# Performance work log

Hardware: AMD Instinct MI355X
Metric: run time of the kernel (lower is better)

Reference implementation:

```python
import jax, jax.numpy as jnp
import numpy as np

ATTN_SCALE = 0.12
HEAD_DIM = 128


def _rms_norm(x):
    # F.rms_norm with no weight; eps defaults to machine eps of dtype
    eps = jnp.asarray(jnp.finfo(x.dtype).eps, x.dtype)
    return x * jax.lax.rsqrt(jnp.mean(x * x, axis=-1, keepdims=True) + eps)


def _rope(x):
    # x: [B, T, H, D]; standard rotary over (first-half, second-half) pairs
    T, D = x.shape[1], x.shape[-1]
    half = D // 2
    inv_freq = 1.0 / (10000.0 ** (jnp.arange(half, dtype=jnp.float32) / half))
    ang = jnp.arange(T, dtype=jnp.float32)[:, None] * inv_freq[None, :]  # [T, half]
    cos = jnp.cos(ang)[None, :, None, :].astype(x.dtype)
    sin = jnp.sin(ang)[None, :, None, :].astype(x.dtype)
    x1, x2 = x[..., :half], x[..., half:]
    return jnp.concatenate([x1 * cos - x2 * sin, x1 * sin + x2 * cos], axis=-1)


def setup_inputs() -> dict:
    key = jax.random.key(0)
    ks = jax.random.split(key, 4)
    B, T, dim, H, hd = 4, 2048, 1024, 8, HEAD_DIM
    hdim = H * hd
    std = 0.5 * dim ** (-0.5)
    bound = (3.0 ** 0.5) * std
    return {
        "x": jax.random.normal(ks[0], (B, T, dim), jnp.float32),
        "ve": jax.random.normal(ks[1], (B, T, hdim), jnp.float32),
        "qkv_w": jax.random.uniform(ks[2], (3, hdim, dim), jnp.float32, -bound, bound),
        "lambdas": jnp.array([0.5, 0.5], jnp.float32),
        "c_proj_w": jax.random.normal(ks[3], (dim, hdim), jnp.float32) * (hdim ** -0.5),
        "c_proj_b": jnp.zeros((dim,), jnp.float32),
    }


def reference(x, ve, qkv_w, lambdas, c_proj_w, c_proj_b):
    B, T, dim = x.shape
    hdim = qkv_w.shape[1]
    hd = HEAD_DIM
    H = hdim // hd
    # fused QKV projection: [B,T,3,H,hd]
    qkv = jnp.einsum('btd,ehd->bteh', x, qkv_w.reshape(3 * hdim, dim).reshape(3 * H, hd, dim).reshape(3 * hdim // hd, hd, dim))
    qkv = jnp.einsum('btd,fd->btf', x, qkv_w.reshape(3 * hdim, dim)).reshape(B, T, 3, H, hd)
    q, k, v = qkv[:, :, 0], qkv[:, :, 1], qkv[:, :, 2]  # each [B,T,H,hd]
    q, k = _rms_norm(q), _rms_norm(k)
    q, k = _rope(q), _rope(k)
    v = lambdas[0] * v + lambdas[1] * ve.reshape(B, T, H, hd)
    # causal SDPA with custom scale
    scores = jnp.einsum('bthd,bshd->bhts', q, k) * ATTN_SCALE  # [B,H,T,T]
    causal = jnp.tril(jnp.ones((T, T), dtype=bool))
    scores = jnp.where(causal[None, None], scores, jnp.finfo(scores.dtype).min)
    p = jax.nn.softmax(scores, axis=-1)
    y = jnp.einsum('bhts,bshd->bthd', p, v).reshape(B, T, hdim)
    return y @ c_proj_w.T + c_proj_b
```

## Files before the change

### kernel.cpp

```cpp
#include <hip/hip_runtime.h>
#include <math.h>

typedef unsigned short u16;
typedef short bf16x8 __attribute__((ext_vector_type(8)));
typedef u16 u16x2 __attribute__((ext_vector_type(2)));
typedef u16 u16x4 __attribute__((ext_vector_type(4)));
typedef u16 u16x8 __attribute__((ext_vector_type(8)));
typedef float f32x2 __attribute__((ext_vector_type(2)));
typedef float f32x4 __attribute__((ext_vector_type(4)));
typedef float f32x16 __attribute__((ext_vector_type(16)));

typedef __attribute__((address_space(1))) const void gvoid_t;
typedef __attribute__((address_space(3))) void lvoid_t;

__device__ __forceinline__ u16 f2bf(float f) {
  union { float f; unsigned u; } v; v.f = f;
  unsigned r = v.u + 0x7fffu + ((v.u >> 16) & 1u);
  return (u16)(r >> 16);
}
__device__ __forceinline__ float bf2f(u16 h) {
  union { unsigned u; float f; } v; v.u = ((unsigned)h) << 16;
  return v.f;
}
__device__ __forceinline__ f32x4 mfma16(bf16x8 a, bf16x8 b, f32x4 c) {
  return __builtin_amdgcn_mfma_f32_16x16x32_bf16(a, b, c, 0, 0, 0);
}
__device__ __forceinline__ f32x16 mfma32(bf16x8 a, bf16x8 b, f32x16 c) {
  return __builtin_amdgcn_mfma_f32_32x32x16_bf16(a, b, c, 0, 0, 0);
}
__device__ __forceinline__ void gload_lds16(const void* g, void* l) {
  __builtin_amdgcn_global_load_lds((gvoid_t*)g, (lvoid_t*)l, 16, 0, 0);
}
__device__ __forceinline__ unsigned cvtpk_bf16(float lo, float hi) {
  unsigned r;
  asm("v_cvt_pk_bf16_f32 %0, %1, %2" : "=v"(r) : "v"(lo), "v"(hi));
  return r;
}
__device__ __forceinline__ void pswap32(unsigned& a, unsigned& b) {
  asm("v_permlane32_swap_b32 %0, %1" : "+v"(a), "+v"(b));
}

__global__ __launch_bounds__(256) void cvt_bf16_kernel(const float* __restrict__ in,
                                                       u16* __restrict__ out, int n4) {
  int i = blockIdx.x * 256 + threadIdx.x;
  if (i >= n4) return;
  f32x4 v = *(const f32x4*)(in + (size_t)i * 4);
  u16x4 o;
  o[0] = f2bf(v[0]); o[1] = f2bf(v[1]); o[2] = f2bf(v[2]); o[3] = f2bf(v[3]);
  *(u16x4*)(out + (size_t)i * 4) = o;
}

__global__ __launch_bounds__(256) void rope_tab_kernel(float* __restrict__ ct,
                                                       float* __restrict__ st) {
  int i = blockIdx.x * 256 + threadIdx.x;
  int t = i >> 6, j = i & 63;
  float inv = powf(10000.f, -(float)j * (1.0f / 64.0f));
  float ang = (float)t * inv;
  ct[i] = cosf(ang);
  st[i] = sinf(ang);
}

template <int OUTF32>
__global__ __launch_bounds__(256) void gemm_bt_kernel(
    const u16* __restrict__ A, const u16* __restrict__ B, void* __restrict__ C,
    const float* __restrict__ bias, int M, int N, int K, int ntn) {
  constexpr int BK = 64;
  __shared__ u16 Alds[128 * BK];
  __shared__ u16 Blds[128 * BK];
  int bid = blockIdx.x;
  int per_g = 8 * ntn;
  int g = bid / per_g, ing = bid % per_g;
  int bm = g * 8 + (ing & 7), bn = ing >> 3;
  size_t m0 = (size_t)bm * 128, n0 = (size_t)bn * 128;
  int tid = threadIdx.x, wid = tid >> 6, lane = tid & 63;
  int wr = wid >> 1, wc = wid & 1, l15 = lane & 15, l4 = lane >> 4;
  int srow = lane >> 3, sch = lane & 7;

  f32x4 acc[4][4];
#pragma unroll
  for (int a = 0; a < 4; a++)
#pragma unroll
    for (int b2 = 0; b2 < 4; b2++) acc[a][b2] = f32x4{0.f, 0.f, 0.f, 0.f};

  int nk = K >> 6;
  for (int kt = 0; kt < nk; ++kt) {
    int k0 = kt << 6;
    __syncthreads();
    const u16* ga = A + (m0 + 32 * wid + srow) * K + k0 + sch * 8;
    const u16* gb = B + (n0 + 32 * wid + srow) * K + k0 + sch * 8;
#pragma unroll
    for (int c = 0; c < 4; c++) {
      gload_lds16(ga + (size_t)(8 * c) * K, &Alds[(32 * wid + 8 * c) * BK]);
      gload_lds16(gb + (size_t)(8 * c) * K, &Blds[(32 * wid + 8 * c) * BK]);
    }
    __syncthreads();
#pragma unroll
    for (int kk = 0; kk < 2; kk++) {
      bf16x8 af[4], bfr[4];
#pragma unroll
      for (int mi = 0; mi < 4; mi++)
        af[mi] = *(const bf16x8*)&Alds[(64 * wr + 16 * mi + l15) * BK + kk * 32 + 8 * l4];
#pragma unroll
      for (int ni = 0; ni < 4; ni++)
        bfr[ni] = *(const bf16x8*)&Blds[(64 * wc + 16 * ni + l15) * BK + kk * 32 + 8 * l4];
#pragma unroll
      for (int mi = 0; mi < 4; mi++)
#pragma unroll
        for (int ni = 0; ni < 4; ni++)
          acc[mi][ni] = mfma16(af[mi], bfr[ni], acc[mi][ni]);
    }
  }
#pragma unroll
  for (int mi = 0; mi < 4; mi++) {
#pragma unroll
    for (int ni = 0; ni < 4; ni++) {
      size_t row = m0 + 64 * wr + 16 * mi + 4 * l4;
      size_t col = n0 + 64 * wc + 16 * ni + l15;
#pragma unroll
      for (int i = 0; i < 4; i++) {
        float v = acc[mi][ni][i];
        if constexpr (OUTF32) {
          ((float*)C)[(row + i) * N + col] = v + bias[col];
        } else {
          ((u16*)C)[(row + i) * N + col] = f2bf(v);
        }
      }
    }
  }
}

__global__ __launch_bounds__(256) void transform_kernel(
    const u16* __restrict__ qkv, const float* __restrict__ ve,
    const float* __restrict__ lam, const float* __restrict__ ct,
    const float* __restrict__ st, u16* __restrict__ qn, u16* __restrict__ kn,
    u16* __restrict__ vt) {
  constexpr int T = 2048, HD = 128;
  __shared__ u16 vtile[64][132];
  int tt = blockIdx.x, bh = blockIdx.y;
  int b = bh >> 3, h = bh & 7;
  int tid = threadIdx.x, wid = tid >> 6, lane = tid & 63;
  float l0 = lam[0], l1 = lam[1];
  int d0 = 2 * lane;
  float sgn = (lane < 32) ? -1.f : 1.f;
#pragma unroll 1
  for (int j = 0; j < 16; ++j) {
    int tl = wid * 16 + j;
    int t = tt * 64 + tl;
    size_t base = ((size_t)(b * T + t)) * 3072 + h * HD + d0;
    u16x2 qraw = *(const u16x2*)(qkv + base);
    u16x2 kraw = *(const u16x2*)(qkv + base + 1024);
    u16x2 vraw = *(const u16x2*)(qkv + base + 2048);
    f32x2 vef = *(const f32x2*)(ve + ((size_t)(b * T + t)) * 1024 + h * HD + d0);
    float q0 = bf2f(qraw[0]), q1 = bf2f(qraw[1]);
    float k0 = bf2f(kraw[0]), k1 = bf2f(kraw[1]);
    float sq = q0 * q0 + q1 * q1, sk = k0 * k0 + k1 * k1;
#pragma unroll
    for (int m = 1; m < 64; m <<= 1) {
      sq += __shfl_xor(sq, m);
      sk += __shfl_xor(sk, m);
    }
    float qs = rsqrtf(sq * (1.f / 128.f) + 1.1920929e-7f);
    float ks = rsqrtf(sk * (1.f / 128.f) + 1.1920929e-7f);
    q0 *= qs; q1 *= qs; k0 *= ks; k1 *= ks;
    int jj = d0 & 63;
    f32x2 c2 = *(const f32x2*)(ct + t * 64 + jj);
    f32x2 s2 = *(const f32x2*)(st + t * 64 + jj);
    float q0p = __shfl_xor(q0, 32), q1p = __shfl_xor(q1, 32);
    float k0p = __shfl_xor(k0, 32), k1p = __shfl_xor(k1, 32);
    u16x2 oq, ok;
    oq[0] = f2bf(q0 * c2[0] + sgn * q0p * s2[0]);
    oq[1] = f2bf(q1 * c2[1] + sgn * q1p * s2[1]);
    ok[0] = f2bf(k0 * c2[0] + sgn * k0p * s2[0]);
    ok[1] = f2bf(k1 * c2[1] + sgn * k1p * s2[1]);
    size_t orow = ((size_t)bh * T + t) * HD + d0;
    *(u16x2*)(qn + orow) = oq;
    *(u16x2*)(kn + orow) = ok;
    vtile[tl][d0] = f2bf(l0 * bf2f(vraw[0]) + l1 * vef[0]);
    vtile[tl][d0 + 1] = f2bf(l0 * bf2f(vraw[1]) + l1 * vef[1]);
  }
  __syncthreads();
#pragma unroll
  for (int it = 0; it < 4; ++it) {
    int ci = it * 256 + tid;
    int d = ci >> 3, c8 = ci & 7;
    u16x8 o;
#pragma unroll
    for (int u = 0; u < 8; u++) o[u] = vtile[c8 * 8 + u][d];
    *(u16x8*)(vt + ((size_t)bh * HD + d) * T + tt * 64 + c8 * 8) = o;
  }
}

__global__ __launch_bounds__(256, 2) void attn_kernel(
    const u16* __restrict__ Qn, const u16* __restrict__ Kn,
    const u16* __restrict__ Vt, u16* __restrict__ Y) {
  constexpr int T = 2048;
  __shared__ u16 Klds[2][64 * 128];
  __shared__ u16 Vlds[2][128 * 64];
  int bid = blockIdx.x;
  int s = 15 - (bid >> 5);
  int bh = bid & 31;
  int b = bh >> 3, h = bh & 7;
  int tid = threadIdx.x, wid = tid >> 6, lane = tid & 63;
  int l31 = lane & 31, hh = lane >> 5;
  const u16* Qb = Qn + (size_t)bh * T * 128;
  const u16* Kb = Kn + (size_t)bh * T * 128;
  const u16* Vb = Vt + (size_t)bh * 128 * T;
  int q0w = s * 128 + wid * 32;
  int qmaxw = q0w + 31;
  int ktend = 2 * s + 2;
  int qg = q0w + l31;

  bf16x8 qf[8];
  {
    const u16* qr = Qb + (size_t)(q0w + l31) * 128 + 8 * hh;
#pragma unroll
    for (int ks = 0; ks < 8; ks++) qf[ks] = *(const bf16x8*)(qr + 16 * ks);
  }
  f32x16 acc[4];
#pragma unroll
  for (int mt = 0; mt < 4; mt++)
#pragma unroll
    for (int r = 0; r < 16; r++) acc[mt][r] = 0.f;
  float m_run = -1e30f, l_run = 0.f;

  auto stage = [&](int buf, int kt) {
#pragma unroll
    for (int it = 0; it < 4; ++it) {
      int id = wid * 256 + it * 64 + lane;
      int r = id >> 4, c = id & 15;
      gload_lds16(Kb + (size_t)(kt * 64 + r) * 128 + 8 * (c ^ (r & 7)),
                  &Klds[buf][(size_t)(wid * 256 + it * 64) * 8]);
      int rv = id >> 3, cv = id & 7;
      gload_lds16(Vb + (size_t)rv * T + kt * 64 + 8 * (cv ^ (rv & 7)),
                  &Vlds[buf][(size_t)(wid * 256 + it * 64) * 8]);
    }
  };

  stage(0, 0);
  __syncthreads();

  for (int kt = 0; kt < ktend; ++kt) {
    int cur = kt & 1;
    if (kt + 1 < ktend) stage(cur ^ 1, kt + 1);
    if (kt * 64 <= qmaxw) {
      const char* kb = (const char*)&Klds[cur][0];
      const char* vb = (const char*)&Vlds[cur][0];
      int rswz = (l31 & 7) << 4;
      f32x16 st0, st1;
#pragma unroll
      for (int r = 0; r < 16; r++) { st0[r] = 0.f; st1[r] = 0.f; }
#pragma unroll
      for (int ks = 0; ks < 8; ks++) {
        bf16x8 kf0 = *(const bf16x8*)(kb + ((l31 * 256 + 32 * ks + 16 * hh) ^ rswz));
        bf16x8 kf1 = *(const bf16x8*)(kb + (((32 + l31) * 256 + 32 * ks + 16 * hh) ^ rswz));
        st0 = mfma32(kf0, qf[ks], st0);
        st1 = mfma32(kf1, qf[ks], st1);
      }
      bool edge = (kt == (qmaxw >> 6));
      if (edge) {
#pragma unroll
        for (int r = 0; r < 16; r++) {
          int kvb = kt * 64 + (r & 3) + 8 * (r >> 2) + 4 * hh;
          st0[r] = (kvb > qg) ? -1e30f : st0[r] * 0.12f;
          st1[r] = (kvb + 32 > qg) ? -1e30f : st1[r] * 0.12f;
        }
      } else {
#pragma unroll
        for (int r = 0; r < 16; r++) { st0[r] *= 0.12f; st1[r] *= 0.12f; }
      }
      float m8[8];
#pragma unroll
      for (int r = 0; r < 8; r++)
        m8[r] = fmaxf(fmaxf(st0[r], st0[r + 8]), fmaxf(st1[r], st1[r + 8]));
#pragma unroll
      for (int r = 0; r < 4; r++) m8[r] = fmaxf(m8[r], m8[r + 4]);
      float pm = fmaxf(fmaxf(m8[0], m8[1]), fmaxf(m8[2], m8[3]));
      pm = fmaxf(pm, __shfl_xor(pm, 32));
      float mnew = fmaxf(m_run, pm);
      float alpha = __expf(m_run - mnew);
      m_run = mnew;
      float sa = 0.f, sb = 0.f, sc = 0.f, sd = 0.f;
#pragma unroll
      for (int r = 0; r < 4; r++) {
        st0[r]      = __expf(st0[r]      - mnew); sa += st0[r];
        st0[r + 4]  = __expf(st0[r + 4]  - mnew); sb += st0[r + 4];
        st0[r + 8]  = __expf(st0[r + 8]  - mnew); sc += st0[r + 8];
        st0[r + 12] = __expf(st0[r + 12] - mnew); sd += st0[r + 12];
        st1[r]      = __expf(st1[r]      - mnew); sa += st1[r];
        st1[r + 4]  = __expf(st1[r + 4]  - mnew); sb += st1[r + 4];
        st1[r + 8]  = __expf(st1[r + 8]  - mnew); sc += st1[r + 8];
        st1[r + 12] = __expf(st1[r + 12] - mnew); sd += st1[r + 12];
      }
      float ps = (sa + sb) + (sc + sd);
      ps += __shfl_xor(ps, 32);
      l_run = l_run * alpha + ps;
#pragma unroll
      for (int mt = 0; mt < 4; mt++)
#pragma unroll
        for (int r = 0; r < 16; r++) acc[mt][r] *= alpha;
      unsigned pA0[4], pB0[4], pA1[4], pB1[4];
#pragma unroll
      for (int rr = 0; rr < 4; rr++) {
        pA0[rr] = cvtpk_bf16(st0[4 * rr], st0[4 * rr + 1]);
        pB0[rr] = cvtpk_bf16(st0[4 * rr + 2], st0[4 * rr + 3]);
        pA1[rr] = cvtpk_bf16(st1[4 * rr], st1[4 * rr + 1]);
        pB1[rr] = cvtpk_bf16(st1[4 * rr + 2], st1[4 * rr + 3]);
      }
      bf16x8 pf[4];
#pragma unroll
      for (int ks2 = 0; ks2 < 4; ks2++) {
        int k1 = ks2 & 1;
        unsigned a0, b0, a1, b1;
        if (ks2 < 2) { a0 = pA0[2 * k1]; b0 = pA0[2 * k1 + 1]; a1 = pB0[2 * k1]; b1 = pB0[2 * k1 + 1]; }
        else         { a0 = pA1[2 * k1]; b0 = pA1[2 * k1 + 1]; a1 = pB1[2 * k1]; b1 = pB1[2 * k1 + 1]; }
        pswap32(a0, b0);
        pswap32(a1, b1);
        union { unsigned w[4]; bf16x8 v; } u;
        u.w[0] = a0; u.w[1] = a1; u.w[2] = b0; u.w[3] = b1;
        pf[ks2] = u.v;
      }
#pragma unroll
      for (int mt = 0; mt < 4; mt++) {
        int row = 32 * mt + l31;
#pragma unroll
        for (int ks2 = 0; ks2 < 4; ks2++) {
          bf16x8 vf = *(const bf16x8*)(vb + ((row * 128 + 32 * ks2 + 16 * hh) ^ rswz));
          acc[mt] = mfma32(vf, pf[ks2], acc[mt]);
        }
      }
    }
    __syncthreads();
  }
  float linv = 1.f / l_run;
  size_t yrow = (size_t)b * T + q0w + l31;
  u16* yp = Y + yrow * 1024 + h * 128;
#pragma unroll
  for (int mt = 0; mt < 4; mt++) {
#pragma unroll
    for (int rr = 0; rr < 4; rr++) {
      u16x4 o;
#pragma unroll
      for (int i = 0; i < 4; i++) o[i] = f2bf(acc[mt][4 * rr + i] * linv);
      *(u16x4*)(yp + 32 * mt + 8 * rr + 4 * hh) = o;
    }
  }
}

extern "C" void kernel_launch(void* const* d_in, const int* in_sizes, int n_in,
                              void* d_out, int out_size, void* d_ws, size_t ws_size,
                              hipStream_t stream) {
  (void)in_sizes; (void)n_in; (void)out_size; (void)ws_size;
  const float* x = (const float*)d_in[0];
  const float* ve = (const float*)d_in[1];
  const float* qkvw = (const float*)d_in[2];
  const float* lam = (const float*)d_in[3];
  const float* cpw = (const float*)d_in[4];
  const float* cpb = (const float*)d_in[5];
  float* out = (float*)d_out;
  char* ws = (char*)d_ws;

  u16* xb   = (u16*)(ws + 0);
  u16* wqkv = (u16*)(ws + 16777216);
  u16* wp   = (u16*)(ws + 23068672);
  u16* qkv  = (u16*)(ws + 25165824);
  u16* qn   = (u16*)(ws + 75497472);
  u16* kn   = (u16*)(ws + 92274688);
  u16* vt   = (u16*)(ws + 109051904);
  float* ctab = (float*)(ws + 125829120);
  float* stab = (float*)(ws + 126353408);
  u16* y = xb;

  rope_tab_kernel<<<512, 256, 0, stream>>>(ctab, stab);
  cvt_bf16_kernel<<<8192, 256, 0, stream>>>(x, xb, 2097152);
  cvt_bf16_kernel<<<3072, 256, 0, stream>>>(qkvw, wqkv, 786432);
  cvt_bf16_kernel<<<1024, 256, 0, stream>>>(cpw, wp, 262144);
  gemm_bt_kernel<0><<<1536, 256, 0, stream>>>(xb, wqkv, qkv, nullptr, 8192, 3072, 1024, 24);
  transform_kernel<<<dim3(32, 32), 256, 0, stream>>>(qkv, ve, lam, ctab, stab, qn, kn, vt);
  attn_kernel<<<512, 256, 0, stream>>>(qn, kn, vt, y);
  gemm_bt_kernel<1><<<512, 256, 0, stream>>>(y, wp, out, cpb, 8192, 1024, 1024, 8);
}
```

Baseline: 226.7 us.

## Replace GEMM with 256x256 double-buffered 8-wave pipelined kernel with swizzled LDS

Rewrites the QKV and output-projection GEMMs as a 512-thread kernel with 256x256 tiles, double-buffered LDS, and interleaved prefetch of the next K tile with MFMA quadrants under explicit waitcnt and barrier control. LDS rows are XOR-swizzled to avoid bank conflicts, and workgroups are remapped in an XCD-aware order. The goal is to hide global load latency and raise data reuse per tile. In exchange it uses 128KB of LDS and more registers, and the output GEMM gets only 128 workgroups, which may underfill the GPU.

```diff
diff --git a/kernel.cpp b/kernel.cpp
--- a/kernel.cpp
+++ b/kernel.cpp
@@ -40,6 +40,17 @@
   asm("v_permlane32_swap_b32 %0, %1" : "+v"(a), "+v"(b));
 }
 
+#define BAR() __builtin_amdgcn_s_barrier()
+#define WAITLGKM()                          \
+  asm volatile("s_waitcnt lgkmcnt(0)");     \
+  __builtin_amdgcn_sched_barrier(0)
+#define WAITVM2()                           \
+  asm volatile("s_waitcnt vmcnt(2)");       \
+  __builtin_amdgcn_sched_barrier(0)
+#define WAITVM4()                           \
+  asm volatile("s_waitcnt vmcnt(4)");       \
+  __builtin_amdgcn_sched_barrier(0)
+
 __global__ __launch_bounds__(256) void cvt_bf16_kernel(const float* __restrict__ in,
                                                        u16* __restrict__ out, int n4) {
   int i = blockIdx.x * 256 + threadIdx.x;
@@ -61,63 +72,125 @@
 }
 
 template <int OUTF32>
-__global__ __launch_bounds__(256) void gemm_bt_kernel(
+__global__ __launch_bounds__(512, 2) void gemm8p_kernel(
     const u16* __restrict__ A, const u16* __restrict__ B, void* __restrict__ C,
-    const float* __restrict__ bias, int M, int N, int K, int ntn) {
-  constexpr int BK = 64;
-  __shared__ u16 Alds[128 * BK];
-  __shared__ u16 Blds[128 * BK];
+    const float* __restrict__ bias, int M, int N, int K, int nbn) {
+  __shared__ u16 Alds[2][256 * 64];
+  __shared__ u16 Blds[2][256 * 64];
+  int nwg = gridDim.x;
+  int cpx = nwg >> 3;
   int bid = blockIdx.x;
-  int per_g = 8 * ntn;
-  int g = bid / per_g, ing = bid % per_g;
-  int bm = g * 8 + (ing & 7), bn = ing >> 3;
-  size_t m0 = (size_t)bm * 128, n0 = (size_t)bn * 128;
+  int swz = (bid & 7) * cpx + (bid >> 3);
+  int bm = swz / nbn, bn = swz % nbn;
+  size_t m0 = (size_t)bm * 256, n0 = (size_t)bn * 256;
   int tid = threadIdx.x, wid = tid >> 6, lane = tid & 63;
-  int wr = wid >> 1, wc = wid & 1, l15 = lane & 15, l4 = lane >> 4;
-  int srow = lane >> 3, sch = lane & 7;
-
-  f32x4 acc[4][4];
-#pragma unroll
-  for (int a = 0; a < 4; a++)
-#pragma unroll
-    for (int b2 = 0; b2 < 4; b2++) acc[a][b2] = f32x4{0.f, 0.f, 0.f, 0.f};
+  int wr = wid >> 2, wc = wid & 3, l15 = lane & 15, l4 = lane >> 4;
+  int srow = tid >> 3, sch = tid & 7;
+
+  const u16* Abase = A + m0 * K;
+  const u16* Bbase = B + n0 * K;
+
+  f32x4 acc[8][4];
+#pragma unroll
+  for (int m = 0; m < 8; m++)
+#pragma unroll
+    for (int n = 0; n < 4; n++) acc[m][n] = f32x4{0.f, 0.f, 0.f, 0.f};
+
+  auto stageA = [&](int buf, int kt, int half) {
+#pragma unroll
+    for (int r = 0; r < 2; ++r) {
+      int row = 128 * half + 64 * r + srow;
+      gload_lds16(Abase + (size_t)row * K + kt * 64 + 8 * (sch ^ (row & 7)),
+                  &Alds[buf][(128 * half + 64 * r + 8 * wid) * 64]);
+    }
+  };
+  auto stageB = [&](int buf, int kt, int half) {
+#pragma unroll
+    for (int r = 0; r < 2; ++r) {
+      int row = 128 * half + 64 * r + srow;
+      gload_lds16(Bbase + (size_t)row * K + kt * 64 + 8 * (sch ^ (row & 7)),
+                  &Blds[buf][(128 * half + 64 * r + 8 * wid) * 64]);
+    }
+  };
+  auto rdA = [&](int buf, int half, bf16x8 (&a)[4][2]) {
+#pragma unroll
+    for (int mi = 0; mi < 4; ++mi)
+#pragma unroll
+      for (int kk = 0; kk < 2; ++kk) {
+        int row = 128 * wr + 64 * half + 16 * mi + l15;
+        a[mi][kk] = *(const bf16x8*)((const char*)(&Alds[buf][0]) + row * 128 +
+                                     ((kk * 64 + 16 * l4) ^ ((row & 7) << 4)));
+      }
+  };
+  auto rdB = [&](int buf, int half, bf16x8 (&bb)[2][2]) {
+#pragma unroll
+    for (int ni = 0; ni < 2; ++ni)
+#pragma unroll
+      for (int kk = 0; kk < 2; ++kk) {
+        int row = 64 * wc + 32 * half + 16 * ni + l15;
+        bb[ni][kk] = *(const bf16x8*)((const char*)(&Blds[buf][0]) + row * 128 +
+                                      ((kk * 64 + 16 * l4) ^ ((row & 7) << 4)));
+      }
+  };
+
+#define QUAD(AF, BF, MH, NH)                                              \
+  do {                                                                    \
+    __builtin_amdgcn_s_setprio(1);                                        \
+    _Pragma("unroll") for (int mi = 0; mi < 4; ++mi)                      \
+        _Pragma("unroll") for (int ni = 0; ni < 2; ++ni)                  \
+            _Pragma("unroll") for (int kk = 0; kk < 2; ++kk)              \
+                acc[4 * MH + mi][2 * NH + ni] =                           \
+        mfma16(AF[mi][kk], BF[ni][kk], acc[4 * MH + mi][2 * NH + ni]);    \
+    __builtin_amdgcn_s_setprio(0);                                        \
+  } while (0)
+
+  stageB(0, 0, 0);
+  stageB(0, 0, 1);
+  stageA(0, 0, 0);
+  stageA(0, 0, 1);
+  WAITVM2();
+  BAR();
 
   int nk = K >> 6;
-  for (int kt = 0; kt < nk; ++kt) {
-    int k0 = kt << 6;
-    __syncthreads();
-    const u16* ga = A + (m0 + 32 * wid + srow) * K + k0 + sch * 8;
-    const u16* gb = B + (n0 + 32 * wid + srow) * K + k0 + sch * 8;
-#pragma unroll
-    for (int c = 0; c < 4; c++) {
-      gload_lds16(ga + (size_t)(8 * c) * K, &Alds[(32 * wid + 8 * c) * BK]);
-      gload_lds16(gb + (size_t)(8 * c) * K, &Blds[(32 * wid + 8 * c) * BK]);
-    }
-    __syncthreads();
-#pragma unroll
-    for (int kk = 0; kk < 2; kk++) {
-      bf16x8 af[4], bfr[4];
-#pragma unroll
-      for (int mi = 0; mi < 4; mi++)
-        af[mi] = *(const bf16x8*)&Alds[(64 * wr + 16 * mi + l15) * BK + kk * 32 + 8 * l4];
-#pragma unroll
-      for (int ni = 0; ni < 4; ni++)
-        bfr[ni] = *(const bf16x8*)&Blds[(64 * wc + 16 * ni + l15) * BK + kk * 32 + 8 * l4];
-#pragma unroll
-      for (int mi = 0; mi < 4; mi++)
-#pragma unroll
-        for (int ni = 0; ni < 4; ni++)
-          acc[mi][ni] = mfma16(af[mi], bfr[ni], acc[mi][ni]);
-    }
-  }
-#pragma unroll
-  for (int mi = 0; mi < 4; mi++) {
-#pragma unroll
-    for (int ni = 0; ni < 4; ni++) {
-      size_t row = m0 + 64 * wr + 16 * mi + 4 * l4;
+  bf16x8 a0[4][2], a1[4][2], b0[2][2], b1[2][2];
+  for (int t = 0; t < nk; ++t) {
+    int buf = t & 1, nxt = buf ^ 1;
+    bool pf = (t + 1 < nk);
+    rdA(buf, 0, a0);
+    rdB(buf, 0, b0);
+    if (pf) stageB(nxt, t + 1, 0);
+    BAR();
+    WAITLGKM();
+    QUAD(a0, b0, 0, 0);
+    BAR();
+    rdB(buf, 1, b1);
+    if (pf) stageB(nxt, t + 1, 1);
+    BAR();
+    WAITLGKM();
+    QUAD(a0, b1, 0, 1);
+    WAITVM4();
+    BAR();
+    rdA(buf, 1, a1);
+    if (pf) stageA(nxt, t + 1, 0);
+    BAR();
+    WAITLGKM();
+    QUAD(a1, b0, 1, 0);
+    BAR();
+    if (pf) stageA(nxt, t + 1, 1);
+    BAR();
+    QUAD(a1, b1, 1, 1);
+    WAITVM2();
+    BAR();
+  }
+
+#pragma unroll
+  for (int mi = 0; mi < 8; ++mi) {
+#pragma unroll
+    for (int ni = 0; ni < 4; ++ni) {
+      size_t row = m0 + 128 * wr + 16 * mi + 4 * l4;
       size_t col = n0 + 64 * wc + 16 * ni + l15;
 #pragma unroll
-      for (int i = 0; i < 4; i++) {
+      for (int i = 0; i < 4; ++i) {
         float v = acc[mi][ni][i];
         if constexpr (OUTF32) {
           ((float*)C)[(row + i) * N + col] = v + bias[col];
@@ -127,6 +200,7 @@
       }
     }
   }
+#undef QUAD
 }
 
 __global__ __launch_bounds__(256) void transform_kernel(
@@ -374,8 +448,8 @@
   cvt_bf16_kernel<<<8192, 256, 0, stream>>>(x, xb, 2097152);
   cvt_bf16_kernel<<<3072, 256, 0, stream>>>(qkvw, wqkv, 786432);
   cvt_bf16_kernel<<<1024, 256, 0, stream>>>(cpw, wp, 262144);
-  gemm_bt_kernel<0><<<1536, 256, 0, stream>>>(xb, wqkv, qkv, nullptr, 8192, 3072, 1024, 24);
+  gemm8p_kernel<0><<<384, 512, 0, stream>>>(xb, wqkv, qkv, nullptr, 8192, 3072, 1024, 12);
   transform_kernel<<<dim3(32, 32), 256, 0, stream>>>(qkv, ve, lam, ctab, stab, qn, kn, vt);
   attn_kernel<<<512, 256, 0, stream>>>(qn, kn, vt, y);
-  gemm_bt_kernel<1><<<512, 256, 0, stream>>>(y, wp, out, cpb, 8192, 1024, 1024, 8);
-}
+  gemm8p_kernel<1><<<128, 512, 0, stream>>>(y, wp, out, cpb, 8192, 1024, 1024, 4);
+}
```

Measured after the change: 209.8 us. 7.5% less time.
